# Kernel optimization log

Measured on AMD Instinct MI355X. Metric: run time of the kernel, lower is better.

Reference implementation:

```python
import jax, jax.numpy as jnp
import numpy as np

# Hyperparameters (from init_kwargs)
N = 100000      # num_nodes
T = 4           # num_edge_type
E = 400000      # edges per type
C = 2           # num_channels
L = 2           # num_layers
W_IN = 128      # input feature dim
D = 64          # node_dim (w_out)
NUM_CLASS = 16
BETA = 0.5
M = 10000       # number of target nodes


def setup_inputs() -> dict:
    key = jax.random.key(0)
    ks = jax.random.split(key, 10)
    glorot = np.sqrt(6.0 / (W_IN + D))
    glorot1 = np.sqrt(6.0 / (C * D + D))
    glorot2 = np.sqrt(6.0 / (D + NUM_CLASS))
    return {
        "X": jax.random.normal(ks[0], (N, W_IN), dtype=jnp.float32),
        "edge_value": jax.random.uniform(ks[1], (T, E), dtype=jnp.float32),
        "conv_weights": 0.1 * jax.random.normal(ks[2], (L, C, T), dtype=jnp.float32),
        "Ws": jax.random.uniform(ks[3], (C, W_IN, D), minval=-glorot, maxval=glorot, dtype=jnp.float32),
        "lin1_w": jax.random.uniform(ks[4], (C * D, D), minval=-glorot1, maxval=glorot1, dtype=jnp.float32),
        "lin1_b": jnp.zeros((D,), dtype=jnp.float32),
        "lin_w": jax.random.uniform(ks[5], (D, NUM_CLASS), minval=-glorot2, maxval=glorot2, dtype=jnp.float32),
        "lin_b": jnp.zeros((NUM_CLASS,), dtype=jnp.float32),
        "edge_index": jax.random.randint(ks[6], (T, 2, E), 0, N),
        "target_x": jax.random.randint(ks[7], (M,), 0, N),
    }


def reference(X, edge_value, conv_weights, Ws, lin1_w, lin1_b, lin_w, lin_b,
              edge_index, target_x):
    # Flatten edge types into one big edge list. torch_sparse.coalesce(op='add')
    # followed by torch.sparse.mm is mathematically a duplicate-summing SpMM,
    # i.e. a segment_sum over destination rows.
    rows = edge_index[:, 0, :].reshape(-1)      # [T*E]
    cols = edge_index[:, 1, :].reshape(-1)      # [T*E]
    vals = edge_value.reshape(-1)               # [T*E]
    type_id = jnp.repeat(jnp.arange(T), E)      # [T*E] edge-type id (constant)

    # Per-channel input projections: X_ = X @ Ws[c]  -> [C, N, D]
    X_ = jnp.einsum('nf,cfd->cnd', X, Ws)
    H = X_

    for l in range(L):
        # FastGTConv: softmax over edge types per channel
        filt = jax.nn.softmax(conv_weights[l], axis=1)   # [C, T]
        newH = []
        for c in range(C):
            v = vals * filt[c, type_id]                  # [T*E] mixed edge weights
            msgs = v[:, None] * H[c][cols]               # gather + scale: [T*E, D]
            newH.append(jax.ops.segment_sum(msgs, rows, num_segments=N))
        H = jnp.stack(newH)                              # [C, N, D]

    # FastGTN tail: relu(beta*X_ + (1-beta)*H), concat channels, linear1
    Hc = jax.nn.relu(BETA * X_ + (1.0 - BETA) * H)       # [C, N, D]
    Hcat = jnp.transpose(Hc, (1, 0, 2)).reshape(N, C * D)
    H_ = Hcat @ lin1_w + lin1_b                          # [N, D]

    # FastGTNs head: logits at target nodes
    return H_[target_x] @ lin_w + lin_b                  # [M, NUM_CLASS]
```

## Files before the change

kernel.cpp:

```cpp
#include <hip/hip_runtime.h>

#define N_NODES   100000
#define T_TYPES   4
#define E_EDGES   400000
#define E4        100000
#define G_TOT     400000
#define TE_TOT    1600000
#define C_CH      2
#define L_LAYERS  2
#define W_INF     128
#define DD        64
#define NUM_CLASS 16
#define BETA      0.5f
#define M_TGT     10000

#define NBKT      196
#define BROWS     512
#define BPAD      9216
#define CHUNK_G   1024
#define NPART_BLK ((G_TOT + CHUNK_G - 1) / CHUNK_G)

static const size_t PLANE2 = (size_t)N_NODES * DD;

typedef __attribute__((ext_vector_type(8))) short short8x;
typedef __attribute__((ext_vector_type(4))) float f32x4;

__device__ __forceinline__ unsigned bf16rne(float x) {
    unsigned u = __float_as_uint(x);
    return (u + 0x7FFFu + ((u >> 16) & 1u)) >> 16;
}
__device__ __forceinline__ unsigned packbf(float a, float b) {
    return bf16rne(a) | (bf16rne(b) << 16);
}
__device__ __forceinline__ float bflo(unsigned u) { return __uint_as_float(u << 16); }
__device__ __forceinline__ float bfhi(unsigned u) { return __uint_as_float(u & 0xFFFF0000u); }

__device__ __forceinline__ void load_filter(const float* cw, int layer,
                                            float* f0, float* f1) {
    float m0 = -1e30f, m1 = -1e30f;
    #pragma unroll
    for (int t = 0; t < T_TYPES; ++t) {
        f0[t] = cw[layer * C_CH * T_TYPES + t];
        f1[t] = cw[layer * C_CH * T_TYPES + T_TYPES + t];
        m0 = fmaxf(m0, f0[t]); m1 = fmaxf(m1, f1[t]);
    }
    float s0 = 0.f, s1 = 0.f;
    #pragma unroll
    for (int t = 0; t < T_TYPES; ++t) {
        f0[t] = __expf(f0[t] - m0); s0 += f0[t];
        f1[t] = __expf(f1[t] - m1); s1 += f1[t];
    }
    #pragma unroll
    for (int t = 0; t < T_TYPES; ++t) { f0[t] /= s0; f1[t] /= s1; }
}

__global__ void wsb_prep(const float* __restrict__ Ws, unsigned short* __restrict__ Wsb) {
    int idx = blockIdx.x * 256 + threadIdx.x;
    if (idx < C_CH * W_INF * DD) {
        int c   = idx >> 13;
        int rem = idx & 8191;
        int d   = rem >> 7;
        int k   = rem & 127;
        Wsb[idx] = (unsigned short)bf16rne(Ws[c * (W_INF * DD) + k * DD + d]);
    }
}

#define AROW 136
__global__ __launch_bounds__(256) void proj_mfma(const float* __restrict__ X,
                                                 const unsigned short* __restrict__ Wsb,
                                                 unsigned* __restrict__ Xp16) {
    __shared__ unsigned short a_lds[64 * AROW];
    int tid  = threadIdx.x;
    int row0 = blockIdx.x * 64;

    const float4* X4 = (const float4*)X;
    #pragma unroll
    for (int i = 0; i < 8; ++i) {
        int gi = tid + 256 * i;
        int r  = gi >> 5;
        int c4 = gi & 31;
        int row = row0 + r;
        float4 v = make_float4(0.f, 0.f, 0.f, 0.f);
        if (row < N_NODES) v = X4[(size_t)row * 32 + c4];
        *(uint2*)&a_lds[r * AROW + c4 * 4] = make_uint2(packbf(v.x, v.y),
                                                        packbf(v.z, v.w));
    }
    __syncthreads();

    int wave = tid >> 6, lane = tid & 63;
    int m = lane & 15, q = lane >> 4;

    short8x A[4];
    #pragma unroll
    for (int ks = 0; ks < 4; ++ks)
        A[ks] = *(const short8x*)&a_lds[(wave * 16 + m) * AROW + ks * 32 + q * 8];

    #pragma unroll
    for (int ct = 0; ct < 4; ++ct) {
        f32x4 acc0 = {0.f, 0.f, 0.f, 0.f};
        f32x4 acc1 = {0.f, 0.f, 0.f, 0.f};
        #pragma unroll
        for (int ks = 0; ks < 4; ++ks) {
            short8x B0 = *(const short8x*)(Wsb + (ct * 16 + m) * 128 + ks * 32 + q * 8);
            short8x B1 = *(const short8x*)(Wsb + 8192 + (ct * 16 + m) * 128 + ks * 32 + q * 8);
            acc0 = __builtin_amdgcn_mfma_f32_16x16x32_bf16(A[ks], B0, acc0, 0, 0, 0);
            acc1 = __builtin_amdgcn_mfma_f32_16x16x32_bf16(A[ks], B1, acc1, 0, 0, 0);
        }
        #pragma unroll
        for (int r = 0; r < 4; ++r) {
            int row = row0 + wave * 16 + q * 4 + r;
            if (row < N_NODES)
                Xp16[(size_t)row * DD + ct * 16 + m] = packbf(acc0[r], acc1[r]);
        }
    }
}

__global__ void init_cursor(int* __restrict__ cursor) {
    int i = threadIdx.x;
    if (i < NBKT) cursor[i] = i * BPAD;
}

__global__ __launch_bounds__(256) void partition_kernel(const int* __restrict__ edge_index,
                                                        const float* __restrict__ edge_value,
                                                        const float* __restrict__ cw,
                                                        int* __restrict__ cursor,
                                                        int4* __restrict__ edata4) {
    __shared__ int cnt[NBKT];
    __shared__ int lbase[NBKT];
    __shared__ int gbase[NBKT];
    __shared__ int2 le[CHUNK_G * 4];
    __shared__ unsigned char lbk[CHUNK_G * 4];
    int tid = threadIdx.x;
    if (tid < NBKT) cnt[tid] = 0;
    __syncthreads();

    float f0[T_TYPES], f1[T_TYPES];
    load_filter(cw, 0, f0, f1);

    int px[16], pv[16], rk[16], bk[16];
    int ne = 0;
    #pragma unroll
    for (int g = 0; g < 4; ++g) {
        int idx = blockIdx.x * CHUNK_G + g * 256 + tid;
        if (idx < G_TOT) {
            int t = idx / E4, r = idx - t * E4;
            const int* bptr = edge_index + (size_t)t * 2 * E_EDGES;
            int4   rw = ((const int4*)bptr)[r];
            int4   cl = ((const int4*)(bptr + E_EDGES))[r];
            float4 vv = ((const float4*)(edge_value + (size_t)t * E_EDGES))[r];
            int tb = t << 17;
            int   rr[4] = {rw.x, rw.y, rw.z, rw.w};
            int   cc[4] = {cl.x, cl.y, cl.z, cl.w};
            float vf[4] = {vv.x, vv.y, vv.z, vv.w};
            #pragma unroll
            for (int k = 0; k < 4; ++k) {
                int b = rr[k] >> 9;
                px[ne] = cc[k] | tb | ((rr[k] & 511) << 19);
                pv[ne] = __float_as_int(vf[k]);
                bk[ne] = b;
                rk[ne] = atomicAdd(&cnt[b], 1);
                ++ne;
            }
        }
    }
    __syncthreads();
    if (tid < 64) {
        int c[4]; int s = 0;
        #pragma unroll
        for (int k = 0; k < 4; ++k) {
            int idx = tid * 4 + k;
            c[k] = (idx < NBKT) ? cnt[idx] : 0;
            s += c[k];
        }
        int inc = s;
        #pragma unroll
        for (int off = 1; off < 64; off <<= 1) {
            int v = __shfl_up(inc, off);
            if (tid >= off) inc += v;
        }
        int base = inc - s;
        #pragma unroll
        for (int k = 0; k < 4; ++k) {
            int idx = tid * 4 + k;
            if (idx < NBKT) lbase[idx] = base;
            base += c[k];
        }
    }
    __syncthreads();
    #pragma unroll
    for (int k = 0; k < 16; ++k) {
        if (k < ne) {
            int slot = lbase[bk[k]] + rk[k];
            le[slot]  = make_int2(px[k], pv[k]);
            lbk[slot] = (unsigned char)bk[k];
        }
    }
    __syncthreads();
    if (tid < NBKT) gbase[tid] = cnt[tid] ? atomicAdd(&cursor[tid], cnt[tid]) : 0;
    __syncthreads();
    int ngrp = min(CHUNK_G, G_TOT - blockIdx.x * CHUNK_G);
    int nloc = 4 * ngrp;
    for (int j = tid; j < nloc; j += 256) {
        int b = lbk[j];
        int2 e = le[j];
        int t = (e.x >> 17) & 3;
        float v = __int_as_float(e.y);
        edata4[gbase[b] + (j - lbase[b])] =
            make_int4(e.x, e.y, __float_as_int(v * f0[t]), __float_as_int(v * f1[t]));
    }
}

__global__ __launch_bounds__(256) void rowsort_kernel(const int* __restrict__ cursor,
                                                      int4* __restrict__ edata4,
                                                      int* __restrict__ offs) {
    __shared__ int rcnt[BROWS];
    __shared__ int rbase[BROWS];
    __shared__ int rcur[BROWS];
    __shared__ int4 le[BPAD];
    int b   = blockIdx.x;
    int tid = threadIdx.x;
    int bb  = b * BPAD;
    int cnt = cursor[b] - bb;
    for (int i = tid; i < BROWS; i += 256) rcnt[i] = 0;
    __syncthreads();
    for (int j = tid; j < cnt; j += 256) {
        int4 e = edata4[bb + j];
        le[j] = e;
        atomicAdd(&rcnt[(e.x >> 19) & 511], 1);
    }
    __syncthreads();
    if (tid < 64) {
        int c[8]; int s = 0;
        #pragma unroll
        for (int k = 0; k < 8; ++k) { c[k] = rcnt[tid * 8 + k]; s += c[k]; }
        int inc = s;
        #pragma unroll
        for (int off = 1; off < 64; off <<= 1) {
            int v = __shfl_up(inc, off);
            if (tid >= off) inc += v;
        }
        int base = inc - s;
        #pragma unroll
        for (int k = 0; k < 8; ++k) { rbase[tid * 8 + k] = base; base += c[k]; }
    }
    __syncthreads();
    for (int i = tid; i < BROWS; i += 256) rcur[i] = rbase[i];
    __syncthreads();
    for (int j = tid; j < cnt; j += 256) {
        int4 e = le[j];
        int lr = (e.x >> 19) & 511;
        int pos = atomicAdd(&rcur[lr], 1);
        edata4[bb + pos] = e;
    }
    int row0  = b * BROWS;
    int nrows = min(BROWS, N_NODES - row0);
    for (int lr = tid; lr < nrows; lr += 256)
        offs[row0 + lr] = bb + rbase[lr] + rcnt[lr];
}

__device__ __forceinline__ void edge_fma(const uint2 h, int wb0, int wb1, float4& acc) {
    float w0 = __int_as_float(wb0), w1 = __int_as_float(wb1);
    acc.x = fmaf(w0, bflo(h.x), acc.x);
    acc.y = fmaf(w1, bfhi(h.x), acc.y);
    acc.z = fmaf(w0, bflo(h.y), acc.z);
    acc.w = fmaf(w1, bfhi(h.y), acc.w);
}

__device__ __forceinline__ void row_gather16(const uint2* __restrict__ hp,
                                             const int4* __restrict__ edata4,
                                             int beg, int end, int slot, int sub,
                                             float4& acc) {
    int i = beg + sub;
    for (; i + 6 < end; i += 8) {
        int4 e0 = edata4[i];
        int4 e1 = edata4[i + 2];
        int4 e2 = edata4[i + 4];
        int4 e3 = edata4[i + 6];
        uint2 h0 = hp[(size_t)((e0.x & 0x1FFFF) * 32 + slot)];
        uint2 h1 = hp[(size_t)((e1.x & 0x1FFFF) * 32 + slot)];
        uint2 h2 = hp[(size_t)((e2.x & 0x1FFFF) * 32 + slot)];
        uint2 h3 = hp[(size_t)((e3.x & 0x1FFFF) * 32 + slot)];
        edge_fma(h0, e0.z, e0.w, acc);
        edge_fma(h1, e1.z, e1.w, acc);
        edge_fma(h2, e2.z, e2.w, acc);
        edge_fma(h3, e3.z, e3.w, acc);
    }
    for (; i < end; i += 2) {
        int4 e = edata4[i];
        uint2 h = hp[(size_t)((e.x & 0x1FFFF) * 32 + slot)];
        edge_fma(h, e.z, e.w, acc);
    }
    acc.x += __shfl_xor(acc.x, 32);
    acc.y += __shfl_xor(acc.y, 32);
    acc.z += __shfl_xor(acc.z, 32);
    acc.w += __shfl_xor(acc.w, 32);
}

__device__ __forceinline__ int row_beg(const int* offs, int row) {
    return ((row & 511) == 0) ? (row >> 9) * BPAD : offs[row - 1];
}

__global__ __launch_bounds__(256) void spmm_gather(const uint2* __restrict__ Hin16,
                                                   uint2* __restrict__ Hout16,
                                                   const int* __restrict__ offs,
                                                   const int4* __restrict__ edata4) {
    int lane = threadIdx.x & 63;
    int slot = lane & 31, sub = lane >> 5;
    int row  = (blockIdx.x * blockDim.x + threadIdx.x) >> 6;
    int beg = row_beg(offs, row);
    int end = offs[row];
    float4 acc = make_float4(0.f, 0.f, 0.f, 0.f);
    row_gather16(Hin16, edata4, beg, end, slot, sub, acc);
    if (sub == 0)
        Hout16[(size_t)row * 32 + slot] = make_uint2(packbf(acc.x, acc.y),
                                                     packbf(acc.z, acc.w));
}

__global__ __launch_bounds__(256) void spmm_gather_tgt(const uint2* __restrict__ Hin16,
                                                       float2* __restrict__ Hout,
                                                       const int* __restrict__ offs,
                                                       const int4* __restrict__ edata4,
                                                       const float* __restrict__ cw,
                                                       const int* __restrict__ tgt) {
    int lane = threadIdx.x & 63;
    int slot = lane & 31, sub = lane >> 5;
    int m    = (blockIdx.x * blockDim.x + threadIdx.x) >> 6;
    float f0[T_TYPES], f1[T_TYPES];
    load_filter(cw, 1, f0, f1);
    int row = tgt[m];
    int beg = row_beg(offs, row);
    int end = offs[row];
    float4 acc = make_float4(0.f, 0.f, 0.f, 0.f);
    for (int i = beg + sub; i < end; i += 2) {
        int4 e = edata4[i];
        int t = (e.x >> 17) & 3;
        float v = __int_as_float(e.y);
        uint2 h = Hin16[(size_t)((e.x & 0x1FFFF) * 32 + slot)];
        float w0 = v * f0[t], w1 = v * f1[t];
        acc.x = fmaf(w0, bflo(h.x), acc.x);
        acc.y = fmaf(w1, bfhi(h.x), acc.y);
        acc.z = fmaf(w0, bflo(h.y), acc.z);
        acc.w = fmaf(w1, bfhi(h.y), acc.w);
    }
    acc.x += __shfl_xor(acc.x, 32);
    acc.y += __shfl_xor(acc.y, 32);
    acc.z += __shfl_xor(acc.z, 32);
    acc.w += __shfl_xor(acc.w, 32);
    if (sub == 0)
        ((float4*)(Hout + (size_t)m * DD))[slot] = acc;
}

__global__ __launch_bounds__(256) void tail_kernel(const unsigned* __restrict__ Xp16,
                                                   const float2* __restrict__ H2,
                                                   const float* __restrict__ lin1_w,
                                                   const float* __restrict__ lin1_b,
                                                   const float* __restrict__ lin_w,
                                                   const float* __restrict__ lin_b,
                                                   const int* __restrict__ tgt,
                                                   float* __restrict__ out) {
    __shared__ float l1w[W_INF * DD];
    __shared__ float lw[DD * NUM_CLASS];
    __shared__ float l1b[DD];
    __shared__ float lb[NUM_CLASS];
    __shared__ float hc[4][W_INF];
    __shared__ float hmid[4][DD];

    int tid = threadIdx.x;
    {
        const float4* g = (const float4*)lin1_w;
        float4* s = (float4*)l1w;
        #pragma unroll
        for (int i = 0; i < 8; ++i) s[tid + 256 * i] = g[tid + 256 * i];
        ((float4*)lw)[tid] = ((const float4*)lin_w)[tid];
        if (tid < DD) l1b[tid] = lin1_b[tid];
        else if (tid < DD + NUM_CLASS) lb[tid - DD] = lin_b[tid - DD];
    }
    __syncthreads();

    int w = tid >> 6, lane = tid & 63;

    #pragma unroll
    for (int g = 0; g < 4; ++g) {
        int m = blockIdx.x * 16 + g * 4 + w;
        int n = tgt[m];
        unsigned xu = Xp16[(size_t)n * DD + lane];
        float2 h  = H2[(size_t)m * DD + lane];
        float a = BETA * bflo(xu) + (1.f - BETA) * h.x;
        float b = BETA * bfhi(xu) + (1.f - BETA) * h.y;
        hc[w][lane]      = fmaxf(a, 0.f);
        hc[w][DD + lane] = fmaxf(b, 0.f);
        __syncthreads();

        float acc = l1b[lane];
        #pragma unroll 8
        for (int k = 0; k < W_INF; ++k)
            acc = fmaf(hc[w][k], l1w[k * DD + lane], acc);
        hmid[w][lane] = acc;
        __syncthreads();

        if (lane < NUM_CLASS) {
            float o = lb[lane];
            #pragma unroll 8
            for (int k = 0; k < DD; ++k)
                o = fmaf(hmid[w][k], lw[k * NUM_CLASS + lane], o);
            out[(size_t)m * NUM_CLASS + lane] = o;
        }
        __syncthreads();
    }
}

extern "C" void kernel_launch(void* const* d_in, const int* in_sizes, int n_in,
                              void* d_out, int out_size, void* d_ws, size_t ws_size,
                              hipStream_t stream) {
    const float* X            = (const float*)d_in[0];
    const float* edge_value   = (const float*)d_in[1];
    const float* conv_weights = (const float*)d_in[2];
    const float* Ws           = (const float*)d_in[3];
    const float* lin1_w       = (const float*)d_in[4];
    const float* lin1_b       = (const float*)d_in[5];
    const float* lin_w        = (const float*)d_in[6];
    const float* lin_b        = (const float*)d_in[7];
    const int*   edge_index   = (const int*)d_in[8];
    const int*   target_x     = (const int*)d_in[9];
    float* out = (float*)d_out;

    float2*         B2   = (float2*)d_ws;
    unsigned*       Xp16 = (unsigned*)(B2 + (size_t)M_TGT * DD);
    unsigned*       H116 = Xp16 + PLANE2;
    unsigned short* Wsb  = (unsigned short*)(H116 + PLANE2);
    int*            offs = (int*)(Wsb + C_CH * W_INF * DD);
    int*            cursor = offs + N_NODES;
    int4*           edata4 = (int4*)(cursor + 256);

    wsb_prep<<<64, 256, 0, stream>>>(Ws, Wsb);
    init_cursor<<<1, 256, 0, stream>>>(cursor);
    partition_kernel<<<NPART_BLK, 256, 0, stream>>>(edge_index, edge_value,
                                                    conv_weights, cursor, edata4);
    proj_mfma<<<(N_NODES + 63) / 64, 256, 0, stream>>>(X, Wsb, Xp16);
    rowsort_kernel<<<NBKT, 256, 0, stream>>>(cursor, edata4, offs);
    spmm_gather<<<(N_NODES * 64) / 256, 256, 0, stream>>>((const uint2*)Xp16,
                                                          (uint2*)H116, offs, edata4);
    spmm_gather_tgt<<<(M_TGT * 64) / 256, 256, 0, stream>>>((const uint2*)H116, B2,
                                                            offs, edata4,
                                                            conv_weights, target_x);
    tail_kernel<<<M_TGT / 16, 256, 0, stream>>>(Xp16, B2, lin1_w, lin1_b, lin_w, lin_b,
                                                target_x, out);
}
```

Baseline: 279.5 us.

## Compress edge records to int2 with bf16 weights, fuse target gather with tail

Edge records shrink from int4 with two fp32 weights to int2 holding a packed pair of bf16 channel weights. This halves the edge traffic in partition, rowsort and the SpMM gather. The layer-2 target gather now rescales the layer-0 weights by a per-type filter ratio and is fused into the tail MLP kernel, which removes the intermediate buffer and a launch. The Wsb prep and cursor init kernels are merged, partition chunks are halved, and rowsort uses 1024-thread blocks. The bf16 edge weights and the ratio trick add rounding error.

```diff
diff --git a/kernel.cpp b/kernel.cpp
--- a/kernel.cpp
+++ b/kernel.cpp
@@ -17,7 +17,7 @@
 #define NBKT      196
 #define BROWS     512
 #define BPAD      9216
-#define CHUNK_G   1024
+#define CHUNK_G   512
 #define NPART_BLK ((G_TOT + CHUNK_G - 1) / CHUNK_G)
 
 static const size_t PLANE2 = (size_t)N_NODES * DD;
@@ -54,14 +54,20 @@
     for (int t = 0; t < T_TYPES; ++t) { f0[t] /= s0; f1[t] /= s1; }
 }
 
-__global__ void wsb_prep(const float* __restrict__ Ws, unsigned short* __restrict__ Wsb) {
-    int idx = blockIdx.x * 256 + threadIdx.x;
-    if (idx < C_CH * W_INF * DD) {
+__global__ void prep_kernel(const float* __restrict__ Ws,
+                            unsigned short* __restrict__ Wsb,
+                            int* __restrict__ cursor) {
+    int b = blockIdx.x;
+    int tid = threadIdx.x;
+    if (b < 64) {
+        int idx = b * 256 + tid;
         int c   = idx >> 13;
         int rem = idx & 8191;
         int d   = rem >> 7;
         int k   = rem & 127;
         Wsb[idx] = (unsigned short)bf16rne(Ws[c * (W_INF * DD) + k * DD + d]);
+    } else {
+        if (tid < NBKT) cursor[tid] = tid * BPAD;
     }
 }
 
@@ -115,16 +121,11 @@
     }
 }
 
-__global__ void init_cursor(int* __restrict__ cursor) {
-    int i = threadIdx.x;
-    if (i < NBKT) cursor[i] = i * BPAD;
-}
-
 __global__ __launch_bounds__(256) void partition_kernel(const int* __restrict__ edge_index,
                                                         const float* __restrict__ edge_value,
                                                         const float* __restrict__ cw,
                                                         int* __restrict__ cursor,
-                                                        int4* __restrict__ edata4) {
+                                                        int2* __restrict__ edata2) {
     __shared__ int cnt[NBKT];
     __shared__ int lbase[NBKT];
     __shared__ int gbase[NBKT];
@@ -137,10 +138,10 @@
     float f0[T_TYPES], f1[T_TYPES];
     load_filter(cw, 0, f0, f1);
 
-    int px[16], pv[16], rk[16], bk[16];
+    int px[8], pv[8], rk[8], bk[8];
     int ne = 0;
     #pragma unroll
-    for (int g = 0; g < 4; ++g) {
+    for (int g = 0; g < 2; ++g) {
         int idx = blockIdx.x * CHUNK_G + g * 256 + tid;
         if (idx < G_TOT) {
             int t = idx / E4, r = idx - t * E4;
@@ -188,7 +189,7 @@
     }
     __syncthreads();
     #pragma unroll
-    for (int k = 0; k < 16; ++k) {
+    for (int k = 0; k < 8; ++k) {
         if (k < ne) {
             int slot = lbase[bk[k]] + rk[k];
             le[slot]  = make_int2(px[k], pv[k]);
@@ -205,26 +206,26 @@
         int2 e = le[j];
         int t = (e.x >> 17) & 3;
         float v = __int_as_float(e.y);
-        edata4[gbase[b] + (j - lbase[b])] =
-            make_int4(e.x, e.y, __float_as_int(v * f0[t]), __float_as_int(v * f1[t]));
-    }
-}
-
-__global__ __launch_bounds__(256) void rowsort_kernel(const int* __restrict__ cursor,
-                                                      int4* __restrict__ edata4,
-                                                      int* __restrict__ offs) {
+        edata2[gbase[b] + (j - lbase[b])] =
+            make_int2(e.x, (int)packbf(v * f0[t], v * f1[t]));
+    }
+}
+
+__global__ __launch_bounds__(1024) void rowsort_kernel(const int* __restrict__ cursor,
+                                                       int2* __restrict__ edata2,
+                                                       int* __restrict__ offs) {
     __shared__ int rcnt[BROWS];
     __shared__ int rbase[BROWS];
     __shared__ int rcur[BROWS];
-    __shared__ int4 le[BPAD];
+    __shared__ int2 le[BPAD];
     int b   = blockIdx.x;
     int tid = threadIdx.x;
     int bb  = b * BPAD;
     int cnt = cursor[b] - bb;
-    for (int i = tid; i < BROWS; i += 256) rcnt[i] = 0;
-    __syncthreads();
-    for (int j = tid; j < cnt; j += 256) {
-        int4 e = edata4[bb + j];
+    if (tid < BROWS) rcnt[tid] = 0;
+    __syncthreads();
+    for (int j = tid; j < cnt; j += 1024) {
+        int2 e = edata2[bb + j];
         le[j] = e;
         atomicAdd(&rcnt[(e.x >> 19) & 511], 1);
     }
@@ -244,58 +245,28 @@
         for (int k = 0; k < 8; ++k) { rbase[tid * 8 + k] = base; base += c[k]; }
     }
     __syncthreads();
-    for (int i = tid; i < BROWS; i += 256) rcur[i] = rbase[i];
-    __syncthreads();
-    for (int j = tid; j < cnt; j += 256) {
-        int4 e = le[j];
+    if (tid < BROWS) rcur[tid] = rbase[tid];
+    __syncthreads();
+    for (int j = tid; j < cnt; j += 1024) {
+        int2 e = le[j];
         int lr = (e.x >> 19) & 511;
         int pos = atomicAdd(&rcur[lr], 1);
-        edata4[bb + pos] = e;
+        edata2[bb + pos] = e;
     }
     int row0  = b * BROWS;
     int nrows = min(BROWS, N_NODES - row0);
-    for (int lr = tid; lr < nrows; lr += 256)
-        offs[row0 + lr] = bb + rbase[lr] + rcnt[lr];
-}
-
-__device__ __forceinline__ void edge_fma(const uint2 h, int wb0, int wb1, float4& acc) {
-    float w0 = __int_as_float(wb0), w1 = __int_as_float(wb1);
+    if (tid < nrows)
+        offs[row0 + tid] = bb + rbase[tid] + rcnt[tid];
+}
+
+__device__ __forceinline__ void edge_fma(const uint2 h, unsigned wp, float4& acc) {
+    float w0 = bflo(wp), w1 = bfhi(wp);
     acc.x = fmaf(w0, bflo(h.x), acc.x);
     acc.y = fmaf(w1, bfhi(h.x), acc.y);
     acc.z = fmaf(w0, bflo(h.y), acc.z);
     acc.w = fmaf(w1, bfhi(h.y), acc.w);
 }
 
-__device__ __forceinline__ void row_gather16(const uint2* __restrict__ hp,
-                                             const int4* __restrict__ edata4,
-                                             int beg, int end, int slot, int sub,
-                                             float4& acc) {
-    int i = beg + sub;
-    for (; i + 6 < end; i += 8) {
-        int4 e0 = edata4[i];
-        int4 e1 = edata4[i + 2];
-        int4 e2 = edata4[i + 4];
-        int4 e3 = edata4[i + 6];
-        uint2 h0 = hp[(size_t)((e0.x & 0x1FFFF) * 32 + slot)];
-        uint2 h1 = hp[(size_t)((e1.x & 0x1FFFF) * 32 + slot)];
-        uint2 h2 = hp[(size_t)((e2.x & 0x1FFFF) * 32 + slot)];
-        uint2 h3 = hp[(size_t)((e3.x & 0x1FFFF) * 32 + slot)];
-        edge_fma(h0, e0.z, e0.w, acc);
-        edge_fma(h1, e1.z, e1.w, acc);
-        edge_fma(h2, e2.z, e2.w, acc);
-        edge_fma(h3, e3.z, e3.w, acc);
-    }
-    for (; i < end; i += 2) {
-        int4 e = edata4[i];
-        uint2 h = hp[(size_t)((e.x & 0x1FFFF) * 32 + slot)];
-        edge_fma(h, e.z, e.w, acc);
-    }
-    acc.x += __shfl_xor(acc.x, 32);
-    acc.y += __shfl_xor(acc.y, 32);
-    acc.z += __shfl_xor(acc.z, 32);
-    acc.w += __shfl_xor(acc.w, 32);
-}
-
 __device__ __forceinline__ int row_beg(const int* offs, int row) {
     return ((row & 511) == 0) ? (row >> 9) * BPAD : offs[row - 1];
 }
@@ -303,61 +274,53 @@
 __global__ __launch_bounds__(256) void spmm_gather(const uint2* __restrict__ Hin16,
                                                    uint2* __restrict__ Hout16,
                                                    const int* __restrict__ offs,
-                                                   const int4* __restrict__ edata4) {
+                                                   const int2* __restrict__ edata2) {
     int lane = threadIdx.x & 63;
     int slot = lane & 31, sub = lane >> 5;
     int row  = (blockIdx.x * blockDim.x + threadIdx.x) >> 6;
     int beg = row_beg(offs, row);
     int end = offs[row];
     float4 acc = make_float4(0.f, 0.f, 0.f, 0.f);
-    row_gather16(Hin16, edata4, beg, end, slot, sub, acc);
-    if (sub == 0)
-        Hout16[(size_t)row * 32 + slot] = make_uint2(packbf(acc.x, acc.y),
-                                                     packbf(acc.z, acc.w));
-}
-
-__global__ __launch_bounds__(256) void spmm_gather_tgt(const uint2* __restrict__ Hin16,
-                                                       float2* __restrict__ Hout,
-                                                       const int* __restrict__ offs,
-                                                       const int4* __restrict__ edata4,
-                                                       const float* __restrict__ cw,
-                                                       const int* __restrict__ tgt) {
-    int lane = threadIdx.x & 63;
-    int slot = lane & 31, sub = lane >> 5;
-    int m    = (blockIdx.x * blockDim.x + threadIdx.x) >> 6;
-    float f0[T_TYPES], f1[T_TYPES];
-    load_filter(cw, 1, f0, f1);
-    int row = tgt[m];
-    int beg = row_beg(offs, row);
-    int end = offs[row];
-    float4 acc = make_float4(0.f, 0.f, 0.f, 0.f);
-    for (int i = beg + sub; i < end; i += 2) {
-        int4 e = edata4[i];
-        int t = (e.x >> 17) & 3;
-        float v = __int_as_float(e.y);
+    int i = beg + sub;
+    for (; i + 6 < end; i += 8) {
+        int2 e0 = edata2[i];
+        int2 e1 = edata2[i + 2];
+        int2 e2 = edata2[i + 4];
+        int2 e3 = edata2[i + 6];
+        uint2 h0 = Hin16[(size_t)((e0.x & 0x1FFFF) * 32 + slot)];
+        uint2 h1 = Hin16[(size_t)((e1.x & 0x1FFFF) * 32 + slot)];
+        uint2 h2 = Hin16[(size_t)((e2.x & 0x1FFFF) * 32 + slot)];
+        uint2 h3 = Hin16[(size_t)((e3.x & 0x1FFFF) * 32 + slot)];
+        edge_fma(h0, (unsigned)e0.y, acc);
+        edge_fma(h1, (unsigned)e1.y, acc);
+        edge_fma(h2, (unsigned)e2.y, acc);
+        edge_fma(h3, (unsigned)e3.y, acc);
+    }
+    for (; i < end; i += 2) {
+        int2 e = edata2[i];
         uint2 h = Hin16[(size_t)((e.x & 0x1FFFF) * 32 + slot)];
-        float w0 = v * f0[t], w1 = v * f1[t];
-        acc.x = fmaf(w0, bflo(h.x), acc.x);
-        acc.y = fmaf(w1, bfhi(h.x), acc.y);
-        acc.z = fmaf(w0, bflo(h.y), acc.z);
-        acc.w = fmaf(w1, bfhi(h.y), acc.w);
+        edge_fma(h, (unsigned)e.y, acc);
     }
     acc.x += __shfl_xor(acc.x, 32);
     acc.y += __shfl_xor(acc.y, 32);
     acc.z += __shfl_xor(acc.z, 32);
     acc.w += __shfl_xor(acc.w, 32);
     if (sub == 0)
-        ((float4*)(Hout + (size_t)m * DD))[slot] = acc;
-}
-
-__global__ __launch_bounds__(256) void tail_kernel(const unsigned* __restrict__ Xp16,
-                                                   const float2* __restrict__ H2,
-                                                   const float* __restrict__ lin1_w,
-                                                   const float* __restrict__ lin1_b,
-                                                   const float* __restrict__ lin_w,
-                                                   const float* __restrict__ lin_b,
-                                                   const int* __restrict__ tgt,
-                                                   float* __restrict__ out) {
+        Hout16[(size_t)row * 32 + slot] = make_uint2(packbf(acc.x, acc.y),
+                                                     packbf(acc.z, acc.w));
+}
+
+__global__ __launch_bounds__(256) void tgt_tail_kernel(const uint2* __restrict__ Hin16,
+                                                       const unsigned* __restrict__ Xp16,
+                                                       const int* __restrict__ offs,
+                                                       const int2* __restrict__ edata2,
+                                                       const float* __restrict__ cw,
+                                                       const int* __restrict__ tgt,
+                                                       const float* __restrict__ lin1_w,
+                                                       const float* __restrict__ lin1_b,
+                                                       const float* __restrict__ lin_w,
+                                                       const float* __restrict__ lin_b,
+                                                       float* __restrict__ out) {
     __shared__ float l1w[W_INF * DD];
     __shared__ float lw[DD * NUM_CLASS];
     __shared__ float l1b[DD];
@@ -375,37 +338,60 @@
         if (tid < DD) l1b[tid] = lin1_b[tid];
         else if (tid < DD + NUM_CLASS) lb[tid - DD] = lin_b[tid - DD];
     }
-    __syncthreads();
+
+    float f0a[T_TYPES], f1a[T_TYPES], f0b[T_TYPES], f1b[T_TYPES];
+    load_filter(cw, 0, f0a, f1a);
+    load_filter(cw, 1, f0b, f1b);
+    float r0[T_TYPES], r1[T_TYPES];
+    #pragma unroll
+    for (int t = 0; t < T_TYPES; ++t) { r0[t] = f0b[t] / f0a[t]; r1[t] = f1b[t] / f1a[t]; }
 
     int w = tid >> 6, lane = tid & 63;
-
-    #pragma unroll
-    for (int g = 0; g < 4; ++g) {
-        int m = blockIdx.x * 16 + g * 4 + w;
-        int n = tgt[m];
-        unsigned xu = Xp16[(size_t)n * DD + lane];
-        float2 h  = H2[(size_t)m * DD + lane];
-        float a = BETA * bflo(xu) + (1.f - BETA) * h.x;
-        float b = BETA * bfhi(xu) + (1.f - BETA) * h.y;
-        hc[w][lane]      = fmaxf(a, 0.f);
-        hc[w][DD + lane] = fmaxf(b, 0.f);
-        __syncthreads();
-
-        float acc = l1b[lane];
+    int slot = lane & 31, sub = lane >> 5;
+    int m = blockIdx.x * 4 + w;
+    int row = tgt[m];
+    int beg = row_beg(offs, row);
+    int end = offs[row];
+    float4 acc = make_float4(0.f, 0.f, 0.f, 0.f);
+    for (int i = beg + sub; i < end; i += 2) {
+        int2 e = edata2[i];
+        int t = (e.x >> 17) & 3;
+        uint2 h = Hin16[(size_t)((e.x & 0x1FFFF) * 32 + slot)];
+        unsigned wp = (unsigned)e.y;
+        float w0 = bflo(wp) * r0[t], w1 = bfhi(wp) * r1[t];
+        acc.x = fmaf(w0, bflo(h.x), acc.x);
+        acc.y = fmaf(w1, bfhi(h.x), acc.y);
+        acc.z = fmaf(w0, bflo(h.y), acc.z);
+        acc.w = fmaf(w1, bfhi(h.y), acc.w);
+    }
+    acc.x += __shfl_xor(acc.x, 32);
+    acc.y += __shfl_xor(acc.y, 32);
+    acc.z += __shfl_xor(acc.z, 32);
+    acc.w += __shfl_xor(acc.w, 32);
+
+    if (sub == 0) {
+        uint2 xu = ((const uint2*)Xp16)[(size_t)row * 32 + slot];
+        int d0 = 2 * slot, d1 = 2 * slot + 1;
+        hc[w][d0]      = fmaxf(BETA * bflo(xu.x) + (1.f - BETA) * acc.x, 0.f);
+        hc[w][DD + d0] = fmaxf(BETA * bfhi(xu.x) + (1.f - BETA) * acc.y, 0.f);
+        hc[w][d1]      = fmaxf(BETA * bflo(xu.y) + (1.f - BETA) * acc.z, 0.f);
+        hc[w][DD + d1] = fmaxf(BETA * bfhi(xu.y) + (1.f - BETA) * acc.w, 0.f);
+    }
+    __syncthreads();
+
+    float a1 = l1b[lane];
+    #pragma unroll 8
+    for (int k = 0; k < W_INF; ++k)
+        a1 = fmaf(hc[w][k], l1w[k * DD + lane], a1);
+    hmid[w][lane] = a1;
+    __syncthreads();
+
+    if (lane < NUM_CLASS) {
+        float o = lb[lane];
         #pragma unroll 8
-        for (int k = 0; k < W_INF; ++k)
-            acc = fmaf(hc[w][k], l1w[k * DD + lane], acc);
-        hmid[w][lane] = acc;
-        __syncthreads();
-
-        if (lane < NUM_CLASS) {
-            float o = lb[lane];
-            #pragma unroll 8
-            for (int k = 0; k < DD; ++k)
-                o = fmaf(hmid[w][k], lw[k * NUM_CLASS + lane], o);
-            out[(size_t)m * NUM_CLASS + lane] = o;
-        }
-        __syncthreads();
+        for (int k = 0; k < DD; ++k)
+            o = fmaf(hmid[w][k], lw[k * NUM_CLASS + lane], o);
+        out[(size_t)m * NUM_CLASS + lane] = o;
     }
 }
 
@@ -424,25 +410,21 @@
     const int*   target_x     = (const int*)d_in[9];
     float* out = (float*)d_out;
 
-    float2*         B2   = (float2*)d_ws;
-    unsigned*       Xp16 = (unsigned*)(B2 + (size_t)M_TGT * DD);
+    unsigned*       Xp16 = (unsigned*)d_ws;
     unsigned*       H116 = Xp16 + PLANE2;
     unsigned short* Wsb  = (unsigned short*)(H116 + PLANE2);
     int*            offs = (int*)(Wsb + C_CH * W_INF * DD);
     int*            cursor = offs + N_NODES;
-    int4*           edata4 = (int4*)(cursor + 256);
-
-    wsb_prep<<<64, 256, 0, stream>>>(Ws, Wsb);
-    init_cursor<<<1, 256, 0, stream>>>(cursor);
+    int2*           edata2 = (int2*)(cursor + 256);
+
+    prep_kernel<<<65, 256, 0, stream>>>(Ws, Wsb, cursor);
     partition_kernel<<<NPART_BLK, 256, 0, stream>>>(edge_index, edge_value,
-                                                    conv_weights, cursor, edata4);
+                                                    conv_weights, cursor, edata2);
     proj_mfma<<<(N_NODES + 63) / 64, 256, 0, stream>>>(X, Wsb, Xp16);
-    rowsort_kernel<<<NBKT, 256, 0, stream>>>(cursor, edata4, offs);
+    rowsort_kernel<<<NBKT, 1024, 0, stream>>>(cursor, edata2, offs);
     spmm_gather<<<(N_NODES * 64) / 256, 256, 0, stream>>>((const uint2*)Xp16,
-                                                          (uint2*)H116, offs, edata4);
-    spmm_gather_tgt<<<(M_TGT * 64) / 256, 256, 0, stream>>>((const uint2*)H116, B2,
-                                                            offs, edata4,
-                                                            conv_weights, target_x);
-    tail_kernel<<<M_TGT / 16, 256, 0, stream>>>(Xp16, B2, lin1_w, lin1_b, lin_w, lin_b,
-                                                target_x, out);
-}
+                                                          (uint2*)H116, offs, edata2);
+    tgt_tail_kernel<<<M_TGT / 4, 256, 0, stream>>>((const uint2*)H116, Xp16, offs,
+                                                   edata2, conv_weights, target_x,
+                                                   lin1_w, lin1_b, lin_w, lin_b, out);
+}
```

Measured after the change: 273.5 us. 1.02x faster.
